# Optimization experiments

Hardware: AMD Instinct MI355X
Metric: run time of the kernel (lower is better)

Reference implementation:

```python
import jax, jax.numpy as jnp
import numpy as np

D_MODEL = 1024
NUM_HEADS = 16
D_K = D_MODEL // NUM_HEADS


def setup_inputs() -> dict:
    key = jax.random.key(0)
    ks = jax.random.split(key, 12)
    B, L, D = 1, 4096, D_MODEL
    s = 1.0 / np.sqrt(D)
    return {
        "q": jax.random.normal(ks[0], (B, L, D), jnp.float32),
        "k": jax.random.normal(ks[1], (B, L, D), jnp.float32),
        "v": jax.random.normal(ks[2], (B, L, D), jnp.float32),
        "wq": jax.random.normal(ks[3], (D, D), jnp.float32) * s,
        "bq": jnp.zeros((D,), jnp.float32),
        "wk": jax.random.normal(ks[4], (D, D), jnp.float32) * s,
        "bk": jnp.zeros((D,), jnp.float32),
        "wv": jax.random.normal(ks[5], (D, D), jnp.float32) * s,
        "bv": jnp.zeros((D,), jnp.float32),
        "wo": jax.random.normal(ks[6], (D, D), jnp.float32) * s,
        "bo": jnp.zeros((D,), jnp.float32),
    }


def reference(q, k, v, wq, bq, wk, bk, wv, bv, wo, bo):
    B, L, D = q.shape
    H, dk = NUM_HEADS, D_K
    # linear projections then split heads: [B, L, D] -> [B, H, L, dk]
    def proj(x, w, b):
        return (x @ w.T + b).reshape(B, L, H, dk).transpose(0, 2, 1, 3)
    qh = proj(q, wq, bq)
    kh = proj(k, wk, bk)
    vh = proj(v, wv, bv)
    scores = jnp.einsum("bhqd,bhkd->bhqk", qh, kh) / jnp.sqrt(jnp.float32(dk))
    attn = jax.nn.softmax(scores, axis=-1)  # [B, H, L, L]
    out = jnp.einsum("bhqk,bhkd->bhqd", attn, vh)
    out = out.transpose(0, 2, 1, 3).reshape(B, L, D)
    return out @ wo.T + bo
```

## Files before the change

kernel.cpp:

```cpp
#include <hip/hip_runtime.h>
#include <hip/hip_bf16.h>
#include <stdint.h>


typedef __bf16 bf16_t;
typedef __bf16 bf16x8 __attribute__((ext_vector_type(8)));
typedef __bf16 bf16x4 __attribute__((ext_vector_type(4)));
typedef float f32x4 __attribute__((ext_vector_type(4)));
typedef unsigned short u16x8 __attribute__((ext_vector_type(8)));

#define MFMA_BF16 __builtin_amdgcn_mfma_f32_16x16x32_bf16

__device__ __forceinline__ void async_copy16(const void* g, void* lds) {
  __builtin_amdgcn_global_load_lds(
      (__attribute__((address_space(1))) void*)(uintptr_t)g,
      (__attribute__((address_space(3))) void*)lds, 16, 0, 0);
}

__global__ __launch_bounds__(256) void cast_f32_bf16(
    const float* __restrict__ s0, bf16_t* __restrict__ d0, int n0,
    const float* __restrict__ s1, bf16_t* __restrict__ d1, int n1,
    const float* __restrict__ s2, bf16_t* __restrict__ d2, int n2,
    const float* __restrict__ s3, bf16_t* __restrict__ d3, int n3,
    const float* __restrict__ s4, bf16_t* __restrict__ d4, int n4,
    const float* __restrict__ s5, bf16_t* __restrict__ d5, int n5,
    const float* __restrict__ s6, bf16_t* __restrict__ d6, int n6) {
  const float* s;
  bf16_t* d;
  int n;
  switch (blockIdx.z) {
    case 0: s = s0; d = d0; n = n0; break;
    case 1: s = s1; d = d1; n = n1; break;
    case 2: s = s2; d = d2; n = n2; break;
    case 3: s = s3; d = d3; n = n3; break;
    case 4: s = s4; d = d4; n = n4; break;
    case 5: s = s5; d = d5; n = n5; break;
    default: s = s6; d = d6; n = n6; break;
  }
  const int i = (blockIdx.x * 256 + threadIdx.x) * 8;
  if (i >= n) return;
  float4 a = *(const float4*)(s + i);
  float4 b = *(const float4*)(s + i + 4);
  bf16x8 o;
  o[0] = (bf16_t)a.x; o[1] = (bf16_t)a.y; o[2] = (bf16_t)a.z; o[3] = (bf16_t)a.w;
  o[4] = (bf16_t)b.x; o[5] = (bf16_t)b.y; o[6] = (bf16_t)b.z; o[7] = (bf16_t)b.w;
  *(bf16x8*)(d + i) = o;
}

__global__ __launch_bounds__(256) void gemm_qkv(
    const bf16_t* __restrict__ A0, const bf16_t* __restrict__ W0,
    const float* __restrict__ b0, bf16_t* __restrict__ D0,
    const bf16_t* __restrict__ A1, const bf16_t* __restrict__ W1,
    const float* __restrict__ b1, bf16_t* __restrict__ D1,
    const bf16_t* __restrict__ A2, const bf16_t* __restrict__ W2,
    const float* __restrict__ b2, bf16_t* __restrict__ D2,
    int M, int N, int K) {
  const bf16_t *A, *W;
  const float* bias;
  bf16_t* D;
  const int zz = blockIdx.z;
  if (zz == 0)      { A = A0; W = W0; bias = b0; D = D0; }
  else if (zz == 1) { A = A1; W = W1; bias = b1; D = D1; }
  else              { A = A2; W = W2; bias = b2; D = D2; }

  __shared__ bf16_t As[128][32];
  __shared__ bf16_t Bs[128][32];

  const int t = threadIdx.x;
  const int w = t >> 6, lane = t & 63;
  const int quad = lane >> 4, l16 = lane & 15;
  const int wr = w >> 1, wc = w & 1;
  const int m0 = blockIdx.x * 128;
  const int n0 = blockIdx.y * 128;
  const int srow = lane >> 2;
  const int scol = (lane & 3) * 8;

  f32x4 acc[4][4] = {};

  for (int k0 = 0; k0 < K; k0 += 32) {
    async_copy16(&A[(size_t)(m0 + (2 * w) * 16 + srow) * K + k0 + scol],
                 (char*)As + (2 * w) * 1024);
    async_copy16(&A[(size_t)(m0 + (2 * w + 1) * 16 + srow) * K + k0 + scol],
                 (char*)As + (2 * w + 1) * 1024);
    async_copy16(&W[(size_t)(n0 + (2 * w) * 16 + srow) * K + k0 + scol],
                 (char*)Bs + (2 * w) * 1024);
    async_copy16(&W[(size_t)(n0 + (2 * w + 1) * 16 + srow) * K + k0 + scol],
                 (char*)Bs + (2 * w + 1) * 1024);
    __syncthreads();

    bf16x8 af[4], bfr[4];
#pragma unroll
    for (int mt = 0; mt < 4; mt++)
      af[mt] = *(const bf16x8*)&As[wr * 64 + mt * 16 + l16][quad * 8];
#pragma unroll
    for (int nt = 0; nt < 4; nt++)
      bfr[nt] = *(const bf16x8*)&Bs[wc * 64 + nt * 16 + l16][quad * 8];
#pragma unroll
    for (int mt = 0; mt < 4; mt++)
#pragma unroll
      for (int nt = 0; nt < 4; nt++)
        acc[mt][nt] = MFMA_BF16(af[mt], bfr[nt], acc[mt][nt], 0, 0, 0);
    __syncthreads();
  }

  if (zz < 2) {
    const float qs = (zz == 0) ? 0.125f * 1.44269504088896340736f : 1.0f;
#pragma unroll
    for (int nt = 0; nt < 4; nt++) {
      const int col = n0 + wc * 64 + nt * 16 + l16;
      const int hh = col >> 6, dk = col & 63;
      const float bb = bias[col];
      const size_t cbase =
          (size_t)hh * 256 * 1024 +
          (size_t)((dk >> 5) * 64 + ((dk >> 3) & 3) * 16) * 8 + (dk & 7);
#pragma unroll
      for (int mt = 0; mt < 4; mt++) {
        const int rowtile = (m0 >> 4) + wr * 4 + mt;
#pragma unroll
        for (int r = 0; r < 4; r++) {
          const int rl = quad * 4 + r;
          D[cbase + (size_t)rowtile * 1024 + rl * 8] =
              (bf16_t)((acc[mt][nt][r] + bb) * qs);
        }
      }
    }
  } else {
#pragma unroll
    for (int nt = 0; nt < 4; nt++) {
      const int col = n0 + wc * 64 + nt * 16 + l16;
      const int hh = col >> 6, dk = col & 63;
      const float bb = bias[col];
#pragma unroll
      for (int mt = 0; mt < 4; mt++) {
        const int kvb = m0 + wr * 64 + mt * 16 + quad * 4;
        const int r50 = kvb & 31;
        bf16x4 pk;
#pragma unroll
        for (int r = 0; r < 4; r++) pk[r] = (bf16_t)(acc[mt][nt][r] + bb);
        const size_t addr =
            (size_t)(hh * 256 + (kvb >> 6) * 4 + (dk >> 4)) * 1024 +
            (size_t)(((kvb >> 5) & 1) * 64 + ((r50 & 15) >> 2) * 16 +
                     (dk & 15)) * 8 +
            (((r50 >> 4) & 1) << 2);
        *(bf16x4*)(D + addr) = pk;
      }
    }
  }
}

__global__ __launch_bounds__(256) void gemm_out(
    const bf16_t* __restrict__ A, const bf16_t* __restrict__ W,
    const float* __restrict__ bias, float* __restrict__ C, int M, int N,
    int K) {
  __shared__ bf16_t As[128][32];
  __shared__ bf16_t Bs[128][32];

  const int t = threadIdx.x;
  const int w = t >> 6, lane = t & 63;
  const int quad = lane >> 4, l16 = lane & 15;
  const int wr = w >> 1, wc = w & 1;
  const int m0 = blockIdx.x * 128;
  const int n0 = blockIdx.y * 128;
  const int srow = lane >> 2;
  const int scol = (lane & 3) * 8;

  f32x4 acc[4][4] = {};

  for (int k0 = 0; k0 < K; k0 += 32) {
    async_copy16(&A[(size_t)(m0 + (2 * w) * 16 + srow) * K + k0 + scol],
                 (char*)As + (2 * w) * 1024);
    async_copy16(&A[(size_t)(m0 + (2 * w + 1) * 16 + srow) * K + k0 + scol],
                 (char*)As + (2 * w + 1) * 1024);
    async_copy16(&W[(size_t)(n0 + (2 * w) * 16 + srow) * K + k0 + scol],
                 (char*)Bs + (2 * w) * 1024);
    async_copy16(&W[(size_t)(n0 + (2 * w + 1) * 16 + srow) * K + k0 + scol],
                 (char*)Bs + (2 * w + 1) * 1024);
    __syncthreads();

    bf16x8 af[4], bfr[4];
#pragma unroll
    for (int mt = 0; mt < 4; mt++)
      af[mt] = *(const bf16x8*)&As[wr * 64 + mt * 16 + l16][quad * 8];
#pragma unroll
    for (int nt = 0; nt < 4; nt++)
      bfr[nt] = *(const bf16x8*)&Bs[wc * 64 + nt * 16 + l16][quad * 8];
#pragma unroll
    for (int mt = 0; mt < 4; mt++)
#pragma unroll
      for (int nt = 0; nt < 4; nt++)
        acc[mt][nt] = MFMA_BF16(af[mt], bfr[nt], acc[mt][nt], 0, 0, 0);
    __syncthreads();
  }

#pragma unroll
  for (int nt = 0; nt < 4; nt++) {
    const int col = n0 + wc * 64 + nt * 16 + l16;
    const float bb = bias[col];
#pragma unroll
    for (int mt = 0; mt < 4; mt++) {
#pragma unroll
      for (int r = 0; r < 4; r++) {
        const int row = m0 + wr * 64 + mt * 16 + quad * 4 + r;
        C[(size_t)row * N + col] = acc[mt][nt][r] + bb;
      }
    }
  }
}

__global__ __launch_bounds__(512, 4) void flash_attn(
    const bf16_t* __restrict__ Qt, const bf16_t* __restrict__ Kt,
    const bf16_t* __restrict__ Vt, bf16_t* __restrict__ O, int L) {
  const int i = blockIdx.x;
  const int slot = i >> 3;
  const int h = (i & 7) * 2 + (slot >> 5);
  const int qblk = slot & 31;

  const int t = threadIdx.x;
  const int w = t >> 6, lane = t & 63;
  const int quad = lane >> 4, l16 = lane & 15;
  const int g = w >> 2;
  const int ws = w & 3;
  const int tq0 = qblk * 8 + ws * 2;

  __shared__ bf16_t Kst[2][8192];
  __shared__ bf16_t Vst[2][8192];

  const size_t hb = (size_t)h * 256 * 1024;

  union V8 {
    bf16x8 v8;
    bf16x4 v4[2];
  };

  bf16x8 qa[2][2];
#pragma unroll
  for (int qt = 0; qt < 2; qt++)
#pragma unroll
    for (int kc = 0; kc < 2; kc++)
      qa[qt][kc] = *(const bf16x8*)(Qt + hb + (size_t)(tq0 + qt) * 1024 +
                                    kc * 512 + lane * 8);

#define STAGE(mc_, buf_)                                                      \
  {                                                                           \
    const size_t pb_ = hb + (size_t)(mc_) * 8192;                             \
    async_copy16(Kt + pb_ + (size_t)t * 8, (char*)&Kst[buf_][0] + w * 1024);  \
    async_copy16(Kt + pb_ + 4096 + (size_t)t * 8,                             \
                 (char*)&Kst[buf_][0] + 8192 + w * 1024);                     \
    async_copy16(Vt + pb_ + (size_t)t * 8, (char*)&Vst[buf_][0] + w * 1024);  \
    async_copy16(Vt + pb_ + 4096 + (size_t)t * 8,                             \
                 (char*)&Vst[buf_][0] + 8192 + w * 1024);                     \
  }

  f32x4 oT[2][4] = {};
  float ls[2] = {0.f, 0.f};
  const int laneK = lane * 16;
  V8 pb[2][2];

#define PHASE_A(buf_)                                                         \
  {                                                                           \
    const char* Kc = (const char*)&Kst[buf_][0] + g * 8192;                   \
    f32x4 sT[2][4];                                                           \
    __builtin_amdgcn_s_setprio(1);                                            \
    _Pragma("unroll") for (int tt = 0; tt < 4; tt++) {                        \
      const bf16x8 k0 = *(const bf16x8*)(Kc + tt * 2048 + laneK);             \
      const bf16x8 k1 = *(const bf16x8*)(Kc + tt * 2048 + 1024 + laneK);      \
      _Pragma("unroll") for (int qt = 0; qt < 2; qt++) {                      \
        f32x4 z = {0.f, 0.f, 0.f, 0.f};                                       \
        z = MFMA_BF16(k0, qa[qt][0], z, 0, 0, 0);                             \
        z = MFMA_BF16(k1, qa[qt][1], z, 0, 0, 0);                             \
        sT[qt][tt] = z;                                                       \
      }                                                                       \
    }                                                                         \
    __builtin_amdgcn_s_setprio(0);                                            \
    _Pragma("unroll") for (int qt = 0; qt < 2; qt++) {                        \
      _Pragma("unroll") for (int tt = 0; tt < 4; tt++) {                      \
        bf16x4 pk;                                                            \
        float rs = 0.f;                                                       \
        _Pragma("unroll") for (int r = 0; r < 4; r++) {                       \
          const float pv = __builtin_amdgcn_exp2f(sT[qt][tt][r]);             \
          rs += pv;                                                           \
          pk[r] = (bf16_t)pv;                                                 \
        }                                                                     \
        ls[qt] += rs;                                                         \
        pb[qt][tt >> 1].v4[tt & 1] = pk;                                      \
      }                                                                       \
    }                                                                         \
  }

#define PHASE_B(buf_)                                                         \
  {                                                                           \
    const char* Vc = (const char*)&Vst[buf_][0] + g * 8192;                   \
    __builtin_amdgcn_s_setprio(1);                                            \
    _Pragma("unroll") for (int dkt = 0; dkt < 4; dkt++) {                     \
      _Pragma("unroll") for (int kvc = 0; kvc < 2; kvc++) {                   \
        const bf16x8 vv =                                                     \
            *(const bf16x8*)(Vc + dkt * 2048 + kvc * 1024 + laneK);           \
        _Pragma("unroll") for (int qt = 0; qt < 2; qt++)                      \
            oT[qt][dkt] = MFMA_BF16(vv, pb[qt][kvc].v8, oT[qt][dkt], 0, 0, 0);\
      }                                                                       \
    }                                                                         \
    __builtin_amdgcn_s_setprio(0);                                            \
  }

  STAGE(0, 0);

  const int NMC = L / 128;
  for (int mc = 0; mc < NMC - 1; mc++) {
    const int buf = mc & 1;
    asm volatile("s_waitcnt vmcnt(2)" ::: "memory");
    __builtin_amdgcn_s_barrier();
    __builtin_amdgcn_sched_barrier(0);
    STAGE(mc + 1, buf ^ 1);
    PHASE_A(buf);
    asm volatile("s_waitcnt vmcnt(4)" ::: "memory");
    __builtin_amdgcn_s_barrier();
    __builtin_amdgcn_sched_barrier(0);
    PHASE_B(buf);
  }
  {
    const int buf = (NMC - 1) & 1;
    asm volatile("s_waitcnt vmcnt(2)" ::: "memory");
    __builtin_amdgcn_s_barrier();
    __builtin_amdgcn_sched_barrier(0);
    PHASE_A(buf);
    asm volatile("s_waitcnt vmcnt(0)" ::: "memory");
    __builtin_amdgcn_s_barrier();
    __builtin_amdgcn_sched_barrier(0);
    PHASE_B(buf);
  }
#undef STAGE
#undef PHASE_A
#undef PHASE_B

  __syncthreads();
  float* sc0 = (float*)&Kst[0][0];
  float* sc1 = (float*)&Vst[0][0];
  const int sidx = (ws * 64 + lane) * 20;
  if (g == 1) {
#pragma unroll
    for (int dkt = 0; dkt < 4; dkt++) {
      *(f32x4*)(sc0 + sidx + dkt * 4) = oT[0][dkt];
      *(f32x4*)(sc1 + sidx + dkt * 4) = oT[1][dkt];
    }
    sc0[sidx + 16] = ls[0];
    sc1[sidx + 16] = ls[1];
  }
  __syncthreads();
  if (g == 0) {
#pragma unroll
    for (int dkt = 0; dkt < 4; dkt++) {
      oT[0][dkt] += *(const f32x4*)(sc0 + sidx + dkt * 4);
      oT[1][dkt] += *(const f32x4*)(sc1 + sidx + dkt * 4);
    }
    ls[0] += sc0[sidx + 16];
    ls[1] += sc1[sidx + 16];

#pragma unroll
    for (int qt = 0; qt < 2; qt++) {
      float l = ls[qt];
      l += __shfl_xor(l, 16);
      l += __shfl_xor(l, 32);
      const float inv = 1.0f / l;
      const size_t row = (size_t)(tq0 + qt) * 16 + l16;
#pragma unroll
      for (int dkt = 0; dkt < 4; dkt++)
#pragma unroll
        for (int r = 0; r < 4; r++)
          O[row * 1024 + h * 64 + dkt * 16 + quad * 4 + r] =
              (bf16_t)(oT[qt][dkt][r] * inv);
    }
  }
}

extern "C" void kernel_launch(void* const* d_in, const int* in_sizes, int n_in,
                              void* d_out, int out_size, void* d_ws,
                              size_t ws_size, hipStream_t stream) {
  const float* q  = (const float*)d_in[0];
  const float* k  = (const float*)d_in[1];
  const float* v  = (const float*)d_in[2];
  const float* wq = (const float*)d_in[3];
  const float* bq = (const float*)d_in[4];
  const float* wk = (const float*)d_in[5];
  const float* bk = (const float*)d_in[6];
  const float* wv = (const float*)d_in[7];
  const float* bv = (const float*)d_in[8];
  const float* wo = (const float*)d_in[9];
  const float* bo = (const float*)d_in[10];
  float* out = (float*)d_out;

  const int L = 4096, D = 1024;
  const int nLD = L * D;
  const int nDD = D * D;
  bf16_t* p = (bf16_t*)d_ws;
  bf16_t* qb  = p; p += nLD;
  bf16_t* kb  = p; p += nLD;
  bf16_t* vb  = p; p += nLD;
  bf16_t* wqb = p; p += nDD;
  bf16_t* wkb = p; p += nDD;
  bf16_t* wvb = p; p += nDD;
  bf16_t* wob = p; p += nDD;
  bf16_t* Op  = p; p += nLD;
  bf16_t* Qt  = p; p += nLD;
  bf16_t* Kt  = p; p += nLD;
  bf16_t* Vt  = p; p += nLD;

  dim3 blk(256);
  cast_f32_bf16<<<dim3(nLD / (256 * 8), 1, 7), blk, 0, stream>>>(
      q, qb, nLD, k, kb, nLD, v, vb, nLD, wq, wqb, nDD, wk, wkb, nDD,
      wv, wvb, nDD, wo, wob, nDD);
  gemm_qkv<<<dim3(L / 128, D / 128, 3), blk, 0, stream>>>(
      qb, wqb, bq, Qt, kb, wkb, bk, Kt, vb, wvb, bv, Vt, L, D, D);
  flash_attn<<<dim3((L / 128) * 16), dim3(512), 0, stream>>>(Qt, Kt, Vt, Op, L);
  gemm_out<<<dim3(L / 128, D / 128), blk, 0, stream>>>(Op, wob, bo, out, L, D,
                                                       D);
}
```

Baseline: 264.6 us.

## Vectorize Q/K epilogue and attention output stores, collapse pipeline into single loop

For the Q and K projection GEMMs the MFMA operands are swapped so each lane holds four consecutive head-dim values. This lets the epilogue load bias as a float4 and write packed bf16x4 stores instead of scalar 2-byte scatters. The attention output store is likewise packed into bf16x4 writes. The attention main loop is merged into one loop with a single full vmcnt(0) wait and barrier per iteration instead of two partial waits. That reduces synchronization points but may expose more load latency, since the next stage is no longer overlapped with phase A.

After: 276.3 us. 4.4% more time.

```diff
diff --git a/kernel.cpp b/kernel.cpp
--- a/kernel.cpp
+++ b/kernel.cpp
@@ -95,33 +95,38 @@
 #pragma unroll
     for (int nt = 0; nt < 4; nt++)
       bfr[nt] = *(const bf16x8*)&Bs[wc * 64 + nt * 16 + l16][quad * 8];
-#pragma unroll
-    for (int mt = 0; mt < 4; mt++)
-#pragma unroll
-      for (int nt = 0; nt < 4; nt++)
-        acc[mt][nt] = MFMA_BF16(af[mt], bfr[nt], acc[mt][nt], 0, 0, 0);
+    if (zz < 2) {
+#pragma unroll
+      for (int mt = 0; mt < 4; mt++)
+#pragma unroll
+        for (int nt = 0; nt < 4; nt++)
+          acc[mt][nt] = MFMA_BF16(bfr[nt], af[mt], acc[mt][nt], 0, 0, 0);
+    } else {
+#pragma unroll
+      for (int mt = 0; mt < 4; mt++)
+#pragma unroll
+        for (int nt = 0; nt < 4; nt++)
+          acc[mt][nt] = MFMA_BF16(af[mt], bfr[nt], acc[mt][nt], 0, 0, 0);
+    }
     __syncthreads();
   }
 
   if (zz < 2) {
     const float qs = (zz == 0) ? 0.125f * 1.44269504088896340736f : 1.0f;
+    const int hh = (n0 >> 6) + wc;
 #pragma unroll
     for (int nt = 0; nt < 4; nt++) {
-      const int col = n0 + wc * 64 + nt * 16 + l16;
-      const int hh = col >> 6, dk = col & 63;
-      const float bb = bias[col];
-      const size_t cbase =
-          (size_t)hh * 256 * 1024 +
-          (size_t)((dk >> 5) * 64 + ((dk >> 3) & 3) * 16) * 8 + (dk & 7);
+      const int b = nt * 16 + quad * 4;
+      const f32x4 bb4 = *(const f32x4*)&bias[n0 + wc * 64 + b];
+      const int ig = ((b >> 5) * 64 + ((b >> 3) & 3) * 16 + l16) * 8 + (b & 7);
 #pragma unroll
       for (int mt = 0; mt < 4; mt++) {
         const int rowtile = (m0 >> 4) + wr * 4 + mt;
-#pragma unroll
-        for (int r = 0; r < 4; r++) {
-          const int rl = quad * 4 + r;
-          D[cbase + (size_t)rowtile * 1024 + rl * 8] =
-              (bf16_t)((acc[mt][nt][r] + bb) * qs);
-        }
+        bf16x4 pk;
+#pragma unroll
+        for (int r = 0; r < 4; r++)
+          pk[r] = (bf16_t)((acc[mt][nt][r] + bb4[r]) * qs);
+        *(bf16x4*)(D + (size_t)(hh * 256 + rowtile) * 1024 + ig) = pk;
       }
     }
   } else {
@@ -256,81 +261,67 @@
   const int laneK = lane * 16;
   V8 pb[2][2];
 
-#define PHASE_A(buf_)                                                         \
-  {                                                                           \
-    const char* Kc = (const char*)&Kst[buf_][0] + g * 8192;                   \
-    f32x4 sT[2][4];                                                           \
-    __builtin_amdgcn_s_setprio(1);                                            \
-    _Pragma("unroll") for (int tt = 0; tt < 4; tt++) {                        \
-      const bf16x8 k0 = *(const bf16x8*)(Kc + tt * 2048 + laneK);             \
-      const bf16x8 k1 = *(const bf16x8*)(Kc + tt * 2048 + 1024 + laneK);      \
-      _Pragma("unroll") for (int qt = 0; qt < 2; qt++) {                      \
-        f32x4 z = {0.f, 0.f, 0.f, 0.f};                                       \
-        z = MFMA_BF16(k0, qa[qt][0], z, 0, 0, 0);                             \
-        z = MFMA_BF16(k1, qa[qt][1], z, 0, 0, 0);                             \
-        sT[qt][tt] = z;                                                       \
-      }                                                                       \
-    }                                                                         \
-    __builtin_amdgcn_s_setprio(0);                                            \
-    _Pragma("unroll") for (int qt = 0; qt < 2; qt++) {                        \
-      _Pragma("unroll") for (int tt = 0; tt < 4; tt++) {                      \
-        bf16x4 pk;                                                            \
-        float rs = 0.f;                                                       \
-        _Pragma("unroll") for (int r = 0; r < 4; r++) {                       \
-          const float pv = __builtin_amdgcn_exp2f(sT[qt][tt][r]);             \
-          rs += pv;                                                           \
-          pk[r] = (bf16_t)pv;                                                 \
-        }                                                                     \
-        ls[qt] += rs;                                                         \
-        pb[qt][tt >> 1].v4[tt & 1] = pk;                                      \
-      }                                                                       \
-    }                                                                         \
-  }
-
-#define PHASE_B(buf_)                                                         \
-  {                                                                           \
-    const char* Vc = (const char*)&Vst[buf_][0] + g * 8192;                   \
-    __builtin_amdgcn_s_setprio(1);                                            \
-    _Pragma("unroll") for (int dkt = 0; dkt < 4; dkt++) {                     \
-      _Pragma("unroll") for (int kvc = 0; kvc < 2; kvc++) {                   \
-        const bf16x8 vv =                                                     \
-            *(const bf16x8*)(Vc + dkt * 2048 + kvc * 1024 + laneK);           \
-        _Pragma("unroll") for (int qt = 0; qt < 2; qt++)                      \
-            oT[qt][dkt] = MFMA_BF16(vv, pb[qt][kvc].v8, oT[qt][dkt], 0, 0, 0);\
-      }                                                                       \
-    }                                                                         \
-    __builtin_amdgcn_s_setprio(0);                                            \
-  }
-
   STAGE(0, 0);
 
   const int NMC = L / 128;
-  for (int mc = 0; mc < NMC - 1; mc++) {
+  for (int mc = 0; mc < NMC; mc++) {
     const int buf = mc & 1;
-    asm volatile("s_waitcnt vmcnt(2)" ::: "memory");
-    __builtin_amdgcn_s_barrier();
-    __builtin_amdgcn_sched_barrier(0);
-    STAGE(mc + 1, buf ^ 1);
-    PHASE_A(buf);
-    asm volatile("s_waitcnt vmcnt(4)" ::: "memory");
-    __builtin_amdgcn_s_barrier();
-    __builtin_amdgcn_sched_barrier(0);
-    PHASE_B(buf);
-  }
-  {
-    const int buf = (NMC - 1) & 1;
-    asm volatile("s_waitcnt vmcnt(2)" ::: "memory");
-    __builtin_amdgcn_s_barrier();
-    __builtin_amdgcn_sched_barrier(0);
-    PHASE_A(buf);
     asm volatile("s_waitcnt vmcnt(0)" ::: "memory");
     __builtin_amdgcn_s_barrier();
     __builtin_amdgcn_sched_barrier(0);
-    PHASE_B(buf);
+    if (mc + 1 < NMC) STAGE(mc + 1, buf ^ 1);
+
+    const char* Kc = (const char*)&Kst[buf][0] + g * 8192;
+    const char* Vc = (const char*)&Vst[buf][0] + g * 8192;
+
+    f32x4 sT[2][4];
+    __builtin_amdgcn_s_setprio(1);
+#pragma unroll
+    for (int tt = 0; tt < 4; tt++) {
+      const bf16x8 k0 = *(const bf16x8*)(Kc + tt * 2048 + laneK);
+      const bf16x8 k1 = *(const bf16x8*)(Kc + tt * 2048 + 1024 + laneK);
+#pragma unroll
+      for (int qt = 0; qt < 2; qt++) {
+        f32x4 z = {0.f, 0.f, 0.f, 0.f};
+        z = MFMA_BF16(k0, qa[qt][0], z, 0, 0, 0);
+        z = MFMA_BF16(k1, qa[qt][1], z, 0, 0, 0);
+        sT[qt][tt] = z;
+      }
+    }
+    __builtin_amdgcn_s_setprio(0);
+
+#pragma unroll
+    for (int qt = 0; qt < 2; qt++) {
+#pragma unroll
+      for (int tt = 0; tt < 4; tt++) {
+        bf16x4 pk;
+        float rs = 0.f;
+#pragma unroll
+        for (int r = 0; r < 4; r++) {
+          const float pv = __builtin_amdgcn_exp2f(sT[qt][tt][r]);
+          rs += pv;
+          pk[r] = (bf16_t)pv;
+        }
+        ls[qt] += rs;
+        pb[qt][tt >> 1].v4[tt & 1] = pk;
+      }
+    }
+
+    __builtin_amdgcn_s_setprio(1);
+#pragma unroll
+    for (int dkt = 0; dkt < 4; dkt++) {
+#pragma unroll
+      for (int kvc = 0; kvc < 2; kvc++) {
+        const bf16x8 vv =
+            *(const bf16x8*)(Vc + dkt * 2048 + kvc * 1024 + laneK);
+#pragma unroll
+        for (int qt = 0; qt < 2; qt++)
+          oT[qt][dkt] = MFMA_BF16(vv, pb[qt][kvc].v8, oT[qt][dkt], 0, 0, 0);
+      }
+    }
+    __builtin_amdgcn_s_setprio(0);
   }
 #undef STAGE
-#undef PHASE_A
-#undef PHASE_B
 
   __syncthreads();
   float* sc0 = (float*)&Kst[0][0];
@@ -363,11 +354,12 @@
       const float inv = 1.0f / l;
       const size_t row = (size_t)(tq0 + qt) * 16 + l16;
 #pragma unroll
-      for (int dkt = 0; dkt < 4; dkt++)
-#pragma unroll
-        for (int r = 0; r < 4; r++)
-          O[row * 1024 + h * 64 + dkt * 16 + quad * 4 + r] =
-              (bf16_t)(oT[qt][dkt][r] * inv);
+      for (int dkt = 0; dkt < 4; dkt++) {
+        bf16x4 ov;
+#pragma unroll
+        for (int r = 0; r < 4; r++) ov[r] = (bf16_t)(oT[qt][dkt][r] * inv);
+        *(bf16x4*)(O + row * 1024 + h * 64 + dkt * 16 + quad * 4) = ov;
+      }
     }
   }
 }
```
